# Performance work log

Hardware: AMD Instinct MI355X
Metric: run time of the kernel (lower is better)

Reference implementation:

```python
import jax, jax.numpy as jnp
import numpy as np

N, C, H, W = 8, 64, 128, 128
CO, K = 64, 3
BN_EPS = 1e-5
POW_EPS = 1e-12  # keeps |x|**alpha differentiable at 0


def setup_inputs() -> dict:
    key = jax.random.key(0)
    k1, k2, k3, k4 = jax.random.split(key, 4)
    x = jax.random.normal(k1, (N, C, H, W), jnp.float32)
    weight = jax.random.normal(k2, (CO, C, K, K), jnp.float32) * 0.1
    gamma = 1.0 + 0.1 * jax.random.normal(k3, (C,), jnp.float32)
    beta = 0.1 * jax.random.normal(k4, (C,), jnp.float32)
    alpha = jnp.float32(1.0)  # learnable power of PowerActivation (AdderSR)
    return {"x": x, "weight": weight, "gamma": gamma, "beta": beta, "alpha": alpha}


def adder2d(x, weight):
    """AdderNet conv: out[n,co,h,w] = -sum_{ci,kh,kw} |patch - W[co,ci,kh,kw]|."""
    co, ci, kh, kw = weight.shape
    # [N, C*kh*kw, H, W], channel-major feature layout matches weight.reshape(co, -1)
    patches = jax.lax.conv_general_dilated_patches(
        x, (kh, kw), (1, 1), padding=((1, 1), (1, 1)))
    wflat = weight.reshape(co, -1)

    def per_out_channel(w):  # w: [C*kh*kw]
        return -jnp.sum(jnp.abs(patches - w[None, :, None, None]), axis=1)  # [N,H,W]

    out = jax.lax.map(per_out_channel, wflat)  # [CO, N, H, W] (sequential -> bounded memory)
    return jnp.transpose(out, (1, 0, 2, 3))    # [N, CO, H, W]


def reference(x, weight, gamma, beta, alpha):
    y = adder2d(x, weight) + x  # residual add
    # BatchNorm2d in training mode: batch statistics over (N, H, W)
    mean = jnp.mean(y, axis=(0, 2, 3), keepdims=True)
    var = jnp.var(y, axis=(0, 2, 3), keepdims=True)
    y = (y - mean) * jax.lax.rsqrt(var + BN_EPS)
    y = y * gamma[None, :, None, None] + beta[None, :, None, None]
    # PowerActivation: sign(x) * |x|^alpha (learnable alpha)
    return jnp.sign(y) * jnp.power(jnp.abs(y) + POW_EPS, alpha)
```

## Files before the change

### kernel.cpp

```cpp
#include <hip/hip_runtime.h>
#include <math.h>

#define N_   8
#define C_   64
#define H_   128
#define W_   128
#define HW_  (H_ * W_)
#define CHW_ (C_ * HW_)
#define K_   3
#define CI_TILE 8
#define CO_BLK  8
#define N_CG    (C_ / CO_BLK)
#define TILE 16
#define HALO (TILE + 2)
#define XSTRIDE 24
#define WSTRIDE (C_ * K_ * K_)
#define BN_EPS 1e-5
#define POW_EPS 1e-12f

#define MAC_TERM(accv, wjk, xvk) do { float t_;                        \
    asm("v_sub_f32 %1, %2, %3\n\t"                                     \
        "v_add_f32 %0, %0, |%1|"                                       \
        : "+v"(accv), "=&v"(t_)                                        \
        : "s"(wjk), "v"(xvk));                                         \
  } while (0)

__global__ __launch_bounds__(256, 8) void adder_kernel(
    const float* __restrict__ x, const float* __restrict__ weight,
    float* __restrict__ y, double* __restrict__ sums)
{
    __shared__ float sx[CI_TILE][HALO][XSTRIDE];
    __shared__ float red[CO_BLK][2][4];

    const int tx = threadIdx.x & 15;
    const int ty = threadIdx.x >> 4;
    const int tile_h = blockIdx.x >> 3;
    const int tile_w = blockIdx.x & 7;
    const int n   = blockIdx.y;
    const int co0 = blockIdx.z * CO_BLK;
    const int h0 = tile_h * TILE;
    const int w0 = tile_w * TILE;

    float acc[CO_BLK];
#pragma unroll
    for (int j = 0; j < CO_BLK; ++j) acc[j] = 0.f;

    const float* xn = x + n * CHW_;

    for (int cb = 0; cb < C_; cb += CI_TILE) {
        __syncthreads();
        for (int idx = threadIdx.x; idx < CI_TILE * HALO * HALO; idx += 256) {
            int ci  = idx / (HALO * HALO);
            int rem = idx - ci * (HALO * HALO);
            int r   = rem / HALO;
            int cc  = rem - r * HALO;
            int gh  = h0 + r - 1;
            int gw  = w0 + cc - 1;
            float v = 0.f;
            if ((unsigned)gh < (unsigned)H_ && (unsigned)gw < (unsigned)W_)
                v = xn[(cb + ci) * HW_ + gh * W_ + gw];
            sx[ci][r][cc] = v;
        }
        __syncthreads();

#pragma unroll 1
        for (int ci = 0; ci < CI_TILE; ++ci) {
            float xv[9];
#pragma unroll
            for (int kh = 0; kh < 3; ++kh)
#pragma unroll
                for (int kw = 0; kw < 3; ++kw)
                    xv[kh * 3 + kw] = sx[ci][ty + kh][tx + kw];

            const float* wp = weight + co0 * WSTRIDE + (cb + ci) * (K_ * K_);
            float w_s[CO_BLK][9];
#pragma unroll
            for (int j = 0; j < CO_BLK; ++j)
#pragma unroll
                for (int k = 0; k < 9; ++k)
                    w_s[j][k] = wp[j * WSTRIDE + k];

#pragma unroll
            for (int j = 0; j < CO_BLK; ++j)
#pragma unroll
                for (int k = 0; k < 9; ++k)
                    MAC_TERM(acc[j], w_s[j][k], xv[k]);
        }
    }

    const int pix = (h0 + ty) * W_ + (w0 + tx);
    float* yo = y + n * CHW_ + co0 * HW_ + pix;
    const float* xr = xn + co0 * HW_ + pix;
    const int lane = threadIdx.x & 63;
    const int wid  = threadIdx.x >> 6;

#pragma unroll
    for (int j = 0; j < CO_BLK; ++j) {
        float v = -acc[j] + xr[j * HW_];
        yo[j * HW_] = v;
        float s = v, ss = v * v;
#pragma unroll
        for (int off = 32; off > 0; off >>= 1) {
            s  += __shfl_down(s, off);
            ss += __shfl_down(ss, off);
        }
        if (lane == 0) { red[j][0][wid] = s; red[j][1][wid] = ss; }
    }
    __syncthreads();
    if (threadIdx.x < CO_BLK) {
        int j = threadIdx.x;
        float S  = red[j][0][0] + red[j][0][1] + red[j][0][2] + red[j][0][3];
        float SS = red[j][1][0] + red[j][1][1] + red[j][1][2] + red[j][1][3];
        atomicAdd(&sums[co0 + j], (double)S);
        atomicAdd(&sums[C_ + co0 + j], (double)SS);
    }
}

__global__ void finalize_kernel(const double* __restrict__ sums,
                                const float* __restrict__ gamma,
                                const float* __restrict__ beta,
                                float* __restrict__ sc)
{
    const int c = threadIdx.x;
    const double cnt = (double)(N_ * HW_);
    double mean = sums[c] / cnt;
    double var  = sums[C_ + c] / cnt - mean * mean;
    float inv   = (float)(1.0 / sqrt(var + (double)BN_EPS));
    float scale = gamma[c] * inv;
    float shift = beta[c] - (float)mean * scale;
    sc[c]      = scale;
    sc[C_ + c] = shift;
}

__global__ __launch_bounds__(256) void apply_kernel(
    float* __restrict__ y, const float* __restrict__ sc,
    const float* __restrict__ alpha_p)
{
    const int idx = blockIdx.x * 256 + threadIdx.x;
    const float alpha = alpha_p[0];
    const int e0 = idx * 4;
    const int c = (e0 / HW_) & (C_ - 1);
    const float scale = sc[c];
    const float shift = sc[C_ + c];

    float4 v = reinterpret_cast<float4*>(y)[idx];
    float* pv = reinterpret_cast<float*>(&v);
    if (alpha == 1.0f) {
#pragma unroll
        for (int i = 0; i < 4; ++i)
            pv[i] = pv[i] * scale + shift;
    } else {
#pragma unroll
        for (int i = 0; i < 4; ++i) {
            float t = pv[i] * scale + shift;
            float sgn = (t > 0.f) ? 1.f : ((t < 0.f) ? -1.f : 0.f);
            pv[i] = sgn * powf(fabsf(t) + POW_EPS, alpha);
        }
    }
    reinterpret_cast<float4*>(y)[idx] = v;
}

extern "C" void kernel_launch(void* const* d_in, const int* in_sizes, int n_in,
                              void* d_out, int out_size, void* d_ws, size_t ws_size,
                              hipStream_t stream)
{
    const float* x      = (const float*)d_in[0];
    const float* weight = (const float*)d_in[1];
    const float* gamma  = (const float*)d_in[2];
    const float* beta   = (const float*)d_in[3];
    const float* alpha  = (const float*)d_in[4];
    float* out = (float*)d_out;

    double* sums = (double*)d_ws;
    float*  sc   = (float*)((char*)d_ws + 128 * sizeof(double));

    hipMemsetAsync(d_ws, 0, 128 * sizeof(double), stream);

    adder_kernel<<<dim3(64, N_, N_CG), 256, 0, stream>>>(x, weight, out, sums);
    finalize_kernel<<<1, C_, 0, stream>>>(sums, gamma, beta, sc);

    const int n4 = (N_ * CHW_) / 4;
    apply_kernel<<<n4 / 256, 256, 0, stream>>>(out, sc, alpha);
}
```

Measured before the change: 326.3 us.

## Double output channels per block and precompute halo staging offsets

```diff
diff --git a/kernel.cpp b/kernel.cpp
--- a/kernel.cpp
+++ b/kernel.cpp
@@ -9,11 +9,14 @@
 #define CHW_ (C_ * HW_)
 #define K_   3
 #define CI_TILE 8
-#define CO_BLK  8
+#define CO_BLK  16
 #define N_CG    (C_ / CO_BLK)
 #define TILE 16
 #define HALO (TILE + 2)
 #define XSTRIDE 24
+#define CISZ (HALO * XSTRIDE)
+#define NSTG ((CI_TILE * HALO * HALO) / 256)
+#define STG_TAIL (CI_TILE * HALO * HALO - NSTG*256)
 #define WSTRIDE (C_ * K_ * K_)
 #define BN_EPS 1e-5
 #define POW_EPS 1e-12f
@@ -29,7 +32,7 @@
     const float* __restrict__ x, const float* __restrict__ weight,
     float* __restrict__ y, double* __restrict__ sums)
 {
-    __shared__ float sx[CI_TILE][HALO][XSTRIDE];
+    __shared__ float sx[CI_TILE * CISZ];
     __shared__ float red[CO_BLK][2][4];
 
     const int tx = threadIdx.x & 15;
@@ -47,44 +50,69 @@
 
     const float* xn = x + n * CHW_;
 
+    int lds_off[NSTG], g_off[NSTG];
+#pragma unroll
+    for (int it = 0; it < NSTG; ++it) {
+        int idx = threadIdx.x + it * 256;
+        int ci  = idx / (HALO * HALO);
+        int rem = idx - ci * (HALO * HALO);
+        int r   = rem / HALO;
+        int cc  = rem - r * HALO;
+        int gh  = h0 + r - 1;
+        int gw  = w0 + cc - 1;
+        bool ok = ((unsigned)gh < (unsigned)H_) && ((unsigned)gw < (unsigned)W_);
+        lds_off[it] = ci * CISZ + r * XSTRIDE + cc;
+        g_off[it]   = ok ? (ci * HW_ + gh * W_ + gw) : -1;
+    }
+    int tail_lds = -1, tail_g = -1;
+    if (threadIdx.x < STG_TAIL) {
+        int idx = NSTG * 256 + threadIdx.x;
+        int ci  = idx / (HALO * HALO);
+        int rem = idx - ci * (HALO * HALO);
+        int r   = rem / HALO;
+        int cc  = rem - r * HALO;
+        int gh  = h0 + r - 1;
+        int gw  = w0 + cc - 1;
+        bool ok = ((unsigned)gh < (unsigned)H_) && ((unsigned)gw < (unsigned)W_);
+        tail_lds = ci * CISZ + r * XSTRIDE + cc;
+        tail_g   = ok ? (ci * HW_ + gh * W_ + gw) : -1;
+    }
+
     for (int cb = 0; cb < C_; cb += CI_TILE) {
+        const float* xncb = xn + cb * HW_;
         __syncthreads();
-        for (int idx = threadIdx.x; idx < CI_TILE * HALO * HALO; idx += 256) {
-            int ci  = idx / (HALO * HALO);
-            int rem = idx - ci * (HALO * HALO);
-            int r   = rem / HALO;
-            int cc  = rem - r * HALO;
-            int gh  = h0 + r - 1;
-            int gw  = w0 + cc - 1;
-            float v = 0.f;
-            if ((unsigned)gh < (unsigned)H_ && (unsigned)gw < (unsigned)W_)
-                v = xn[(cb + ci) * HW_ + gh * W_ + gw];
-            sx[ci][r][cc] = v;
+#pragma unroll
+        for (int it = 0; it < NSTG; ++it) {
+            float v = (g_off[it] >= 0) ? xncb[g_off[it]] : 0.f;
+            sx[lds_off[it]] = v;
+        }
+        if (tail_lds >= 0) {
+            float v = (tail_g >= 0) ? xncb[tail_g] : 0.f;
+            sx[tail_lds] = v;
         }
         __syncthreads();
 
 #pragma unroll 1
         for (int ci = 0; ci < CI_TILE; ++ci) {
+            const float* sxc = &sx[ci * CISZ];
             float xv[9];
 #pragma unroll
             for (int kh = 0; kh < 3; ++kh)
 #pragma unroll
                 for (int kw = 0; kw < 3; ++kw)
-                    xv[kh * 3 + kw] = sx[ci][ty + kh][tx + kw];
+                    xv[kh * 3 + kw] = sxc[(ty + kh) * XSTRIDE + tx + kw];
 
             const float* wp = weight + co0 * WSTRIDE + (cb + ci) * (K_ * K_);
-            float w_s[CO_BLK][9];
-#pragma unroll
-            for (int j = 0; j < CO_BLK; ++j)
+#pragma unroll
+            for (int j = 0; j < CO_BLK; ++j) {
+                float wj[9];
 #pragma unroll
                 for (int k = 0; k < 9; ++k)
-                    w_s[j][k] = wp[j * WSTRIDE + k];
-
-#pragma unroll
-            for (int j = 0; j < CO_BLK; ++j)
+                    wj[k] = wp[j * WSTRIDE + k];
 #pragma unroll
                 for (int k = 0; k < 9; ++k)
-                    MAC_TERM(acc[j], w_s[j][k], xv[k]);
+                    MAC_TERM(acc[j], wj[k], xv[k]);
+            }
         }
     }
 
```

Result: no change. 325.1 us (-0.4%).
